# Kernel tuning notes

Measured on AMD Instinct MI355X. Metric: run time of the kernel, lower is better.

Reference implementation:

```python
import jax, jax.numpy as jnp
import numpy as np

M = 64    # multiplicity (channels per harmonic degree)
P = 64    # positional encoding dim
EPS = 1e-5


def sinusoidal_pe(N, P):
    pos = jnp.arange(N, dtype=jnp.float32)[:, None]
    div = jnp.exp(jnp.arange(0, P, 2, dtype=jnp.float32) * (-np.log(10000.0) / P))
    pe = jnp.zeros((N, P), dtype=jnp.float32)
    pe = pe.at[:, 0::2].set(jnp.sin(pos * div))
    pe = pe.at[:, 1::2].set(jnp.cos(pos * div))
    return pe


def split_irreps(h):
    # h: [B, N, 4M] -> scalar part [B,N,M], vector part [B,N,M,3]
    B, N, _ = h.shape
    h4 = h.reshape(B, N, M, 4)
    return h4[..., 0], h4[..., 1:]


def merge_irreps(s, v):
    B, N, _ = s.shape
    return jnp.concatenate([s[..., None], v], axis=-1).reshape(B, N, M * 4)


def hyena_block(h, Wq, Wk, Wv, filt, Wo):
    # Hyena-style gated long convolution: q * conv(k * v), FFT circular conv along seq
    N = h.shape[1]
    q = h @ Wq
    k = h @ Wk
    v = h @ Wv
    kf = jnp.fft.rfft(filt, n=N, axis=0)                       # [N//2+1, H]
    conv = jnp.fft.irfft(jnp.fft.rfft(k * v, n=N, axis=1) * kf[None], n=N, axis=1)
    return (q * conv) @ Wo


def reg_linear(h, W0, W1):
    # degree-wise linear mixing across multiplicity (equivariant)
    s, v = split_irreps(h)
    return merge_irreps(jnp.einsum('bnm,mk->bnk', s, W0),
                        jnp.einsum('bnmd,mk->bnkd', v, W1))


def reg_batchnorm(h, g0, g1):
    # normalize per-channel irrep norms over (batch, tokens); learnable per-channel gain
    s, v = split_irreps(h)
    n0 = jnp.sqrt(jnp.mean(s * s, axis=(0, 1)) + EPS)          # [M]
    n1 = jnp.sqrt(jnp.mean(jnp.sum(v * v, axis=-1), axis=(0, 1)) + EPS)
    return merge_irreps(s / n0 * g0, v / n1[:, None] * g1[:, None])


def norm_activation(h):
    # norm-gated nonlinearity: each irrep scaled by sigmoid of its norm (equivariant)
    s, v = split_irreps(h)
    vn = jnp.sqrt(jnp.sum(v * v, axis=-1, keepdims=True) + EPS)
    return merge_irreps(s * jax.nn.sigmoid(jnp.abs(s)), v * jax.nn.sigmoid(vn))


def setup_inputs() -> dict:
    key = jax.random.key(0)
    B, N = 64, 1024
    D = M * 4
    H = [360, 360, 160]   # 10*sum(2l+1,l<=5)=360, 360, 10*sum(2l+1,l<=3)=160
    ks = iter(jax.random.split(key, 64))
    def rn(shape, scale=0.02):
        return jax.random.normal(next(ks), shape, dtype=jnp.float32) * scale
    inp = {
        'x': jax.random.normal(next(ks), (B, N, 3), dtype=jnp.float32),
        'tok_emb': rn((3, P)),
        'Wf': rn((P, M)),
        'wv': rn((M,), 0.5),
        'w_out': rn((M,), 0.5),
    }
    for i, Hi in enumerate(H, start=1):
        inp[f'Wq{i}'] = rn((D, Hi)); inp[f'Wk{i}'] = rn((D, Hi)); inp[f'Wv{i}'] = rn((D, Hi))
        inp[f'filt{i}'] = rn((N, Hi)); inp[f'Wo{i}'] = rn((Hi, D))
        inp[f'Wm0_{i}'] = rn((M, M)); inp[f'Wm1_{i}'] = rn((M, M))
        inp[f'g0_{i}'] = jnp.ones((M,), jnp.float32); inp[f'g1_{i}'] = jnp.ones((M,), jnp.float32)
    return inp


def reference(x, tok_emb, Wf, wv, w_out,
              Wq1, Wk1, Wv1, filt1, Wo1, Wm0_1, Wm1_1, g0_1, g1_1,
              Wq2, Wk2, Wv2, filt2, Wo2, Wm0_2, Wm1_2, g0_2, g1_2,
              Wq3, Wk3, Wv3, filt3, Wo3, Wm0_3, Wm1_3, g0_3, g1_3):
    B, N, _ = x.shape
    # invariant features: sinusoidal PE + token-type embedding (alternating 0/1, last token 2)
    pe = sinusoidal_pe(N, P)
    tt = jnp.arange(N) % 2
    tt = tt.at[-1].set(2)
    f = pe + tok_emb[tt]                                        # [N, P]
    # input conversion: invariants -> degree-0 channels; input vector -> degree-1 channels
    s0 = jnp.broadcast_to((f @ Wf)[None], (B, N, M))
    v0 = x[:, :, None, :] * wv[None, None, :, None]             # [B, N, M, 3]
    h = merge_irreps(s0, v0)                                    # [B, N, 4M]
    layers = [
        (Wq1, Wk1, Wv1, filt1, Wo1, Wm0_1, Wm1_1, g0_1, g1_1),
        (Wq2, Wk2, Wv2, filt2, Wo2, Wm0_2, Wm1_2, g0_2, g1_2),
        (Wq3, Wk3, Wv3, filt3, Wo3, Wm0_3, Wm1_3, g0_3, g1_3),
    ]
    for (Wq, Wk, Wv_, filt, Wo, Wm0, Wm1, g0, g1) in layers:
        h = h + hyena_block(h, Wq, Wk, Wv_, filt, Wo)           # hyena + residual
        y = reg_linear(h, Wm0, Wm1)                             # mlp
        y = reg_batchnorm(y, g0, g1)                            # batch norm
        y = norm_activation(y)                                  # norm activation
        h = h + y                                               # residual
    pooled = h.mean(axis=1)                                     # [B, 4M] mean pool over tokens
    _, vpool = split_irreps(pooled[:, None, :])                 # [B, 1, M, 3]
    return jnp.einsum('bmd,m->bd', vpool[:, 0], w_out)          # [B, 3]
```

## Files before the change

kernel.cpp:

```cpp
#include <hip/hip_runtime.h>
#include <math.h>

namespace {

typedef __bf16 bf16_t;
typedef bf16_t bf16x8 __attribute__((ext_vector_type(8)));
typedef float floatx4 __attribute__((ext_vector_type(4)));

constexpr int kN = 1024;
constexpr int kM = 64;
constexpr int kP = 64;
constexpr float kEps = 1e-5f;
constexpr int kFN = 1024;

__device__ __forceinline__ float sigmoidf(float v) { return 1.0f / (1.0f + expf(-v)); }

__device__ __forceinline__ floatx4 mfma16(bf16x8 a, bf16x8 b, floatx4 c) {
  return __builtin_amdgcn_mfma_f32_16x16x32_bf16(a, b, c, 0, 0, 0);
}

__device__ __forceinline__ void fma3(floatx4& acc, bf16x8 ah, bf16x8 al,
                                     bf16x8 bh, bf16x8 bl) {
  acc = mfma16(ah, bh, acc);
  acc = mfma16(ah, bl, acc);
  acc = mfma16(al, bh, acc);
}

__device__ __forceinline__ void load_split8(const float* p, bf16x8& hi, bf16x8& lo) {
  const float4 u = *(const float4*)p;
  const float4 v = *(const float4*)(p + 4);
  const float a[8] = {u.x, u.y, u.z, u.w, v.x, v.y, v.z, v.w};
#pragma unroll
  for (int i = 0; i < 8; ++i) {
    const bf16_t h_ = (bf16_t)a[i];
    hi[i] = h_;
    lo[i] = (bf16_t)(a[i] - (float)h_);
  }
}

union U4 { uint4 u; bf16_t b[8]; };

__device__ __forceinline__ void glds16(const bf16_t* g, bf16_t* l) {
  __builtin_amdgcn_global_load_lds(
      (const __attribute__((address_space(1))) void*)g,
      (__attribute__((address_space(3))) void*)l, 16, 0, 0);
}

__device__ __forceinline__ size_t hidx(int r, int d8) {
  const int rb = r >> 6, rr = r & 63;
  return (size_t)(rb * 8 + (d8 >> 2)) * 4096 + (rr >> 4) * 1024 + (d8 & 3) * 128 + (rr & 15) * 8;
}

__device__ __forceinline__ int zi(int i) { return i + (i >> 4); }

__device__ __forceinline__ float2 cadd(float2 a, float2 b) { return {a.x + b.x, a.y + b.y}; }
__device__ __forceinline__ float2 csub(float2 a, float2 b) { return {a.x - b.x, a.y - b.y}; }
__device__ __forceinline__ float2 cmul(float2 a, float2 w) {
  return {a.x * w.x - a.y * w.y, a.x * w.y + a.y * w.x};
}
__device__ __forceinline__ float2 cmulc(float2 a, float2 w) {
  return {a.x * w.x + a.y * w.y, a.y * w.x - a.x * w.y};
}

__global__ void k_s0(const float* __restrict__ tok_emb, const float* __restrict__ Wf,
                     float* __restrict__ s0) {
  __shared__ float f[kP];
  const int n = blockIdx.x;
  const int t = threadIdx.x;
  const int tt = (n == kN - 1) ? 2 : (n & 1);
  const int j = t >> 1;
  const float cexp = (float)(-9.210340371976184 / 64.0);
  const float divj = expf((float)(2 * j) * cexp);
  const float ang = (float)n * divj;
  const float pe = (t & 1) ? cosf(ang) : sinf(ang);
  f[t] = pe + tok_emb[tt * kP + t];
  __syncthreads();
  float acc = 0.0f;
#pragma unroll 8
  for (int p = 0; p < kP; ++p) acc = fmaf(f[p], Wf[p * kM + t], acc);
  s0[n * kM + t] = acc;
}

__global__ void k_h0(const float* __restrict__ x, const float* __restrict__ wv,
                     const float* __restrict__ s0, bf16_t* __restrict__ hsh) {
  const int idx = blockIdx.x * 256 + threadIdx.x;
  const int r = idx >> 5, d8 = idx & 31;
  const int n = r & (kN - 1);
  const int m0 = d8 * 2, m1 = m0 + 1;
  const float w0 = wv[m0], w1 = wv[m1];
  const float x0 = x[r * 3 + 0], x1 = x[r * 3 + 1], x2 = x[r * 3 + 2];
  float f[8];
  f[0] = s0[n * kM + m0]; f[1] = x0 * w0; f[2] = x1 * w0; f[3] = x2 * w0;
  f[4] = s0[n * kM + m1]; f[5] = x0 * w1; f[6] = x1 * w1; f[7] = x2 * w1;
  U4 oh, ol;
#pragma unroll
  for (int i = 0; i < 8; ++i) {
    const bf16_t h_ = (bf16_t)f[i];
    oh.b[i] = h_; ol.b[i] = (bf16_t)(f[i] - (float)h_);
  }
  const size_t base = hidx(r, d8);
  *(uint4*)(hsh + base) = oh.u;
  *(uint4*)(hsh + base + 512) = ol.u;
}

__global__ void k_wqkv3(const float* __restrict__ Wq0, const float* __restrict__ Wk0,
                        const float* __restrict__ Wv0,
                        const float* __restrict__ Wq1, const float* __restrict__ Wk1,
                        const float* __restrict__ Wv1,
                        const float* __restrict__ Wq2, const float* __restrict__ Wk2,
                        const float* __restrict__ Wv2, bf16_t* __restrict__ wall3) {
  const int l = blockIdx.y;
  const int H = (l == 2) ? 160 : 360;
  const int gy = (l == 2) ? 3 : 6;
  const int c = blockIdx.x;
  if (c >= gy * 64) return;
  const int k = threadIdx.x;
  const float* Wq = (l == 0) ? Wq0 : ((l == 1) ? Wq1 : Wq2);
  const float* Wk = (l == 0) ? Wk0 : ((l == 1) ? Wk1 : Wk2);
  const float* Wv = (l == 0) ? Wv0 : ((l == 1) ? Wv1 : Wv2);
  bf16_t* wall = wall3 + ((l == 2) ? 1179648 : (size_t)l * 589824);
  const bool ok = c < H;
  const float w[3] = {ok ? Wq[k * H + c] : 0.f, ok ? Wk[k * H + c] : 0.f,
                      ok ? Wv[k * H + c] : 0.f};
  const int ct = c >> 6, cgrp = (c >> 4) & 3, cl = c & 15;
  const int kc = k >> 5, quad = (k >> 3) & 3, off = k & 7;
  const size_t base = (size_t)(ct * 8 + kc) * 12288 + cgrp * 512 + quad * 128 + cl * 8 + off;
#pragma unroll
  for (int mat = 0; mat < 3; ++mat) {
    const bf16_t hi = (bf16_t)w[mat];
    wall[base + mat * 4096] = hi;
    wall[base + mat * 4096 + 2048] = (bf16_t)(w[mat] - (float)hi);
  }
}

__global__ void k_wo3(const float* __restrict__ Wo0, const float* __restrict__ Wo1,
                      const float* __restrict__ Wo2, bf16_t* __restrict__ WoF3) {
  const int l = blockIdx.y;
  const int H = (l == 2) ? 160 : 360;
  const float* Wo = (l == 0) ? Wo0 : ((l == 1) ? Wo1 : Wo2);
  bf16_t* WoF = WoF3 + (size_t)l * 196608;
  const int d = blockIdx.x;
  const int c = threadIdx.x;
  const float w = (c < H) ? Wo[c * 256 + d] : 0.f;
  const int dt = d >> 6, dgrp = (d >> 4) & 3, dl = d & 15;
  const int kc = c >> 5, quad = (c >> 3) & 3, off = c & 7;
  const size_t base = (size_t)(dt * 12 + kc) * 4096 + dgrp * 512 + quad * 128 + dl * 8 + off;
  const bf16_t hi = (bf16_t)w;
  WoF[base] = hi;
  WoF[base + 2048] = (bf16_t)(w - (float)hi);
}

__global__ void k_bt3(const float* __restrict__ W00, const float* __restrict__ W10,
                      const float* __restrict__ W01, const float* __restrict__ W11,
                      const float* __restrict__ W02, const float* __restrict__ W12,
                      bf16_t* __restrict__ BtF3) {
  const int l = blockIdx.y;
  const float* W0 = (l == 0) ? W00 : ((l == 1) ? W01 : W02);
  const float* W1 = (l == 0) ? W10 : ((l == 1) ? W11 : W12);
  bf16_t* BtF = BtF3 + (size_t)l * 131072;
  const int col = blockIdx.x, row = threadIdx.x;
  const int k = col >> 2, ck = col & 3, m = row >> 2, cm = row & 3;
  float v = 0.f;
  if (cm == ck) v = (ck == 0 ? W0 : W1)[m * 64 + k];
  const int ct = col >> 6, cgrp = (col >> 4) & 3, cl = col & 15;
  const int kc = row >> 5, quad = (row >> 3) & 3, off = row & 7;
  const size_t base = (size_t)(ct * 8 + kc) * 4096 + cgrp * 512 + quad * 128 + cl * 8 + off;
  const bf16_t hi = (bf16_t)v;
  BtF[base] = hi;
  BtF[base + 2048] = (bf16_t)(v - (float)hi);
}

__global__ void k_tw(float2* __restrict__ twg) {
  const int j = blockIdx.x * 256 + threadIdx.x;
  if (j < kFN / 2) {
    float s, c;
    sincosf(-6.283185307179586f * (float)j / (float)kFN, &s, &c);
    twg[j].x = c; twg[j].y = s;
  }
}

__device__ void fft_dif(float2* z, const float2* tw) {
  const int p = threadIdx.x;
#pragma unroll
  for (int m = 256; m >= 1; m >>= 2) {
    __syncthreads();
    const int pm = p & (m - 1);
    const int j = ((p & ~(m - 1)) << 2) | pm;
    const int tm2 = 512 / (2 * m), tm1 = 512 / m;
    const float2 x0 = z[zi(j)], x1 = z[zi(j + m)];
    const float2 x2 = z[zi(j + 2 * m)], x3 = z[zi(j + 3 * m)];
    const float2 w2 = tw[pm * tm2], w2b = tw[(pm + m) * tm2], w1 = tw[pm * tm1];
    const float2 a0 = cadd(x0, x2), a2 = cmul(csub(x0, x2), w2);
    const float2 a1 = cadd(x1, x3), a3 = cmul(csub(x1, x3), w2b);
    z[zi(j)]         = cadd(a0, a1);
    z[zi(j + m)]     = cmul(csub(a0, a1), w1);
    z[zi(j + 2 * m)] = cadd(a2, a3);
    z[zi(j + 3 * m)] = cmul(csub(a2, a3), w1);
  }
}

__device__ void fft_dit_inv(float2* z, const float2* tw) {
  const int p = threadIdx.x;
#pragma unroll
  for (int m = 1; m <= 256; m <<= 2) {
    __syncthreads();
    const int pm = p & (m - 1);
    const int j = ((p & ~(m - 1)) << 2) | pm;
    const int tm2 = 512 / (2 * m), tm1 = 512 / m;
    const float2 x0 = z[zi(j)], x1 = z[zi(j + m)];
    const float2 x2 = z[zi(j + 2 * m)], x3 = z[zi(j + 3 * m)];
    const float2 w1 = tw[pm * tm1], w2 = tw[pm * tm2], w2b = tw[(pm + m) * tm2];
    const float2 c1 = cmulc(x1, w1), c3 = cmulc(x3, w1);
    const float2 b0 = cadd(x0, c1), b1 = csub(x0, c1);
    const float2 b2 = cadd(x2, c3), b3 = csub(x2, c3);
    const float2 d2 = cmulc(b2, w2), d3 = cmulc(b3, w2b);
    z[zi(j)]         = cadd(b0, d2);
    z[zi(j + 2 * m)] = csub(b0, d2);
    z[zi(j + m)]     = cadd(b1, d3);
    z[zi(j + 3 * m)] = csub(b1, d3);
  }
}

__global__ __launch_bounds__(256) void k_kf(const float* __restrict__ filt, int H,
                                            const float2* __restrict__ twg,
                                            float2* __restrict__ kf) {
  __shared__ float2 z[kFN + kFN / 16];
  __shared__ float2 tw[kFN / 2];
  const int c = blockIdx.x;
  for (int j = threadIdx.x; j < kFN / 2; j += 256) tw[j] = twg[j];
  for (int n = threadIdx.x; n < kFN; n += 256) {
    z[zi(n)].x = filt[n * H + c];
    z[zi(n)].y = 0.0f;
  }
  fft_dif(z, tw);
  __syncthreads();
  for (int j = threadIdx.x; j < kFN; j += 256) kf[c * kFN + j] = z[zi(j)];
}

__global__ __launch_bounds__(256) void k_conv(float* kvt, const float* __restrict__ qt,
                                              const float2* __restrict__ kf,
                                              const float2* __restrict__ twg, int H) {
  __shared__ float2 z[kFN + kFN / 16];
  __shared__ float2 tw[kFN / 2];
  const int blk = blockIdx.x;
  const int c = blk % H;
  const int pb = blk / H;
  float* sig0 = kvt + (((size_t)((2 * pb) * H + c)) << 10);
  float* sig1 = kvt + (((size_t)((2 * pb + 1) * H + c)) << 10);
  const float* q0 = qt + (((size_t)((2 * pb) * H + c)) << 10);
  const float* q1 = qt + (((size_t)((2 * pb + 1) * H + c)) << 10);
  for (int j = threadIdx.x; j < kFN / 2; j += 256) tw[j] = twg[j];
  for (int n = threadIdx.x; n < kFN; n += 256) {
    z[zi(n)].x = sig0[n];
    z[zi(n)].y = sig1[n];
  }
  fft_dif(z, tw);
  __syncthreads();
  for (int j = threadIdx.x; j < kFN; j += 256) {
    const float2 a = z[zi(j)];
    const float2 b = kf[c * kFN + j];
    float2 o;
    o.x = a.x * b.x - a.y * b.y;
    o.y = a.x * b.y + a.y * b.x;
    z[zi(j)] = o;
  }
  fft_dit_inv(z, tw);
  __syncthreads();
  const float s = 1.0f / (float)kFN;
  for (int n = threadIdx.x; n < kFN; n += 256) {
    sig0[n] = (z[zi(n)].x * s) * q0[n];
    sig1[n] = (z[zi(n)].y * s) * q1[n];
  }
}

__global__ __launch_bounds__(256) void k_qkv(const bf16_t* __restrict__ hsh,
    const bf16_t* __restrict__ wall, int H,
    float* __restrict__ qt, float* __restrict__ kvt) {
  __shared__ bf16_t lds[20480];
  const int gy = (H + 63) >> 6;
  const int bid = blockIdx.x;
  const int xcd = bid & 7, sseq = bid >> 3;
  const int ct = sseq % gy;
  const int rb2 = (sseq / gy) * 8 + xcd;
  const int rb0 = rb2 * 2, rb1 = rb0 + 1;
  const int t = threadIdx.x;
  const int lane = t & 63, wave = t >> 6;
  const int l15 = lane & 15, quad = lane >> 4;
  const int c0 = ct * 64;
  const int wr = (wave & 1) * 32, wc = (wave >> 1) * 32;
  const int wr16 = (wave & 1) * 2, wc16 = (wave >> 1) * 2;
  const int q128l = quad * 128 + l15 * 8;
  floatx4 aq[2][2][2] = {}, ak_[2][2][2] = {}, av_[2][2][2] = {};
  for (int kt = 0; kt < 8; ++kt) {
    {
      const bf16_t* A0 = hsh + (size_t)(rb0 * 8 + kt) * 4096;
      const bf16_t* A1 = hsh + (size_t)(rb1 * 8 + kt) * 4096;
      const bf16_t* Bs = wall + (size_t)(ct * 8 + kt) * 12288;
#pragma unroll
      for (int s = 0; s < 10; ++s) {
        const int seg = wave * 10 + s;
        const bf16_t* src = (seg < 8) ? (A0 + seg * 512)
                          : (seg < 16) ? (A1 + (seg - 8) * 512)
                                       : (Bs + (seg - 16) * 512);
        glds16(src + lane * 8, &lds[seg * 512]);
      }
    }
    __syncthreads();
    bf16x8 ah[2][2], al[2][2];
#pragma unroll
    for (int rbx = 0; rbx < 2; ++rbx)
#pragma unroll
      for (int i = 0; i < 2; ++i) {
        ah[rbx][i] = *(const bf16x8*)(lds + rbx * 4096 + ((wr16 + i) * 2 + 0) * 512 + q128l);
        al[rbx][i] = *(const bf16x8*)(lds + rbx * 4096 + ((wr16 + i) * 2 + 1) * 512 + q128l);
      }
#pragma unroll
    for (int mat = 0; mat < 3; ++mat) {
      const int bb = 8192 + mat * 4096;
#pragma unroll
      for (int j = 0; j < 2; ++j) {
        const bf16x8 bh = *(const bf16x8*)(lds + bb + (wc16 + j) * 512 + q128l);
        const bf16x8 bl = *(const bf16x8*)(lds + bb + 2048 + (wc16 + j) * 512 + q128l);
#pragma unroll
        for (int rbx = 0; rbx < 2; ++rbx)
#pragma unroll
          for (int i = 0; i < 2; ++i) {
            floatx4& a = (mat == 0) ? aq[rbx][i][j]
                       : (mat == 1) ? ak_[rbx][i][j] : av_[rbx][i][j];
            fma3(a, ah[rbx][i], al[rbx][i], bh, bl);
          }
      }
    }
    __syncthreads();
  }
#pragma unroll
  for (int rbx = 0; rbx < 2; ++rbx) {
    const int r0 = (rb0 + rbx) * 64;
    const int b = r0 >> 10;
    const int n0 = r0 & 1023;
#pragma unroll
    for (int j = 0; j < 2; ++j) {
      const int c = c0 + wc + j * 16 + l15;
      if (c < H) {
        const size_t rbw = (((size_t)(b * H + c)) << 10) + n0 + wr + quad * 4;
#pragma unroll
        for (int i = 0; i < 2; ++i) {
          float4 p;
          p.x = aq[rbx][i][j][0]; p.y = aq[rbx][i][j][1];
          p.z = aq[rbx][i][j][2]; p.w = aq[rbx][i][j][3];
          *(float4*)(qt + rbw + i * 16) = p;
        }
#pragma unroll
        for (int i = 0; i < 2; ++i) {
          float4 p;
          p.x = ak_[rbx][i][j][0] * av_[rbx][i][j][0];
          p.y = ak_[rbx][i][j][1] * av_[rbx][i][j][1];
          p.z = ak_[rbx][i][j][2] * av_[rbx][i][j][2];
          p.w = ak_[rbx][i][j][3] * av_[rbx][i][j][3];
          *(float4*)(kvt + rbw + i * 16) = p;
        }
      }
    }
  }
}

__global__ __launch_bounds__(256) void k_mix(const float* __restrict__ pv, int H, int KT,
    const bf16_t* __restrict__ WoF, bf16_t* __restrict__ hsh) {
  __shared__ float smem[4352];
  const int r0 = blockIdx.x * 64;
  const int t = threadIdx.x;
  const int lane = t & 63, wave = t >> 6;
  const int l15 = lane & 15, quad = lane >> 4;
  const int b = r0 >> 10, n0 = r0 & 1023;
  const int wr = (wave & 1) * 32, wh = wave >> 1;
  const int q128l = quad * 128 + l15 * 8;
  floatx4 acc[2][8] = {};
  const int cl = t >> 3, n8 = (t & 7) * 8;
  for (int kt = 0; kt < KT; ++kt) {
    const int ck0 = kt * 32;
    __syncthreads();
    {
      const int c = ck0 + cl;
      float p[8] = {};
      if (c < H) {
        const size_t o = (((size_t)(b * H + c)) << 10) + n0 + n8;
        const float4 p0 = *(const float4*)(pv + o);
        const float4 p1 = *(const float4*)(pv + o + 4);
        p[0] = p0.x; p[1] = p0.y; p[2] = p0.z; p[3] = p0.w;
        p[4] = p1.x; p[5] = p1.y; p[6] = p1.z; p[7] = p1.w;
      }
#pragma unroll
      for (int u = 0; u < 8; ++u) smem[(n8 + u) * 36 + cl] = p[u];
    }
    __syncthreads();
    bf16x8 ah0, al0, ah1, al1;
    load_split8(smem + (wr + l15) * 36 + quad * 8, ah0, al0);
    load_split8(smem + (wr + 16 + l15) * 36 + quad * 8, ah1, al1);
#pragma unroll
    for (int j = 0; j < 8; ++j) {
      const int jj = wh * 8 + j;
      const int dt = jj >> 2, dgrp = jj & 3;
      const bf16_t* Bb = WoF + (size_t)(dt * 12 + kt) * 4096 + dgrp * 512 + q128l;
      const bf16x8 bh = *(const bf16x8*)Bb;
      const bf16x8 bl = *(const bf16x8*)(Bb + 2048);
      fma3(acc[0][j], ah0, al0, bh, bl);
      fma3(acc[1][j], ah1, al1, bh, bl);
    }
  }
  const int nl = t >> 2, q4 = t & 3;
  const int r = r0 + nl;
#pragma unroll
  for (int g = 0; g < 4; ++g) {
    __syncthreads();
    if (wh == (g >> 1)) {
#pragma unroll
      for (int jl = 0; jl < 4; ++jl) {
        const int j = (g & 1) * 4 + jl;
#pragma unroll
        for (int i = 0; i < 2; ++i)
#pragma unroll
          for (int rr = 0; rr < 4; ++rr)
            smem[(wr + i * 16 + quad * 4 + rr) * 68 + jl * 16 + l15] = acc[i][j][rr];
      }
    }
    __syncthreads();
#pragma unroll
    for (int u8 = 0; u8 < 2; ++u8) {
      const int d8 = g * 8 + q4 * 2 + u8;
      const size_t base = hidx(r, d8);
      U4 hi, lo;
      hi.u = *(const uint4*)(hsh + base);
      lo.u = *(const uint4*)(hsh + base + 512);
      U4 oh, ol;
#pragma unroll
      for (int i = 0; i < 8; ++i) {
        const float f = (float)hi.b[i] + (float)lo.b[i] +
                        smem[nl * 68 + (q4 * 2 + u8) * 8 + i];
        const bf16_t h_ = (bf16_t)f;
        oh.b[i] = h_; ol.b[i] = (bf16_t)(f - (float)h_);
      }
      *(uint4*)(hsh + base) = oh.u;
      *(uint4*)(hsh + base + 512) = ol.u;
    }
  }
}

__global__ __launch_bounds__(256) void k_reg(const bf16_t* __restrict__ hsh,
    const bf16_t* __restrict__ BtF,
    float* __restrict__ y, float* __restrict__ partial) {
  __shared__ float smf[6144];
  __shared__ float red[256];
  bf16_t* lds = (bf16_t*)smf;
  const int bid = blockIdx.x;
  const int xcd = bid & 7, sseq = bid >> 3;
  const int ct = sseq & 3;
  const int rb2 = (sseq >> 2) * 8 + xcd;
  const int rb0 = rb2 * 2, rb1 = rb0 + 1;
  const int t = threadIdx.x;
  const int lane = t & 63, wave = t >> 6;
  const int l15 = lane & 15, quad = lane >> 4;
  const int c0 = ct * 64;
  const int wr = (wave & 1) * 32, wc = (wave >> 1) * 32;
  const int wr16 = (wave & 1) * 2, wc16 = (wave >> 1) * 2;
  const int q128l = quad * 128 + l15 * 8;
  floatx4 acc[2][2][2] = {};
  for (int kt = 0; kt < 8; ++kt) {
    {
      const bf16_t* A0 = hsh + (size_t)(rb0 * 8 + kt) * 4096;
      const bf16_t* A1 = hsh + (size_t)(rb1 * 8 + kt) * 4096;
      const bf16_t* Bs = BtF + (size_t)(ct * 8 + kt) * 4096;
#pragma unroll
      for (int s = 0; s < 6; ++s) {
        const int seg = wave * 6 + s;
        const bf16_t* src = (seg < 8) ? (A0 + seg * 512)
                          : (seg < 16) ? (A1 + (seg - 8) * 512)
                                       : (Bs + (seg - 16) * 512);
        glds16(src + lane * 8, &lds[seg * 512]);
      }
    }
    __syncthreads();
    bf16x8 ah[2][2], al[2][2];
#pragma unroll
    for (int rbx = 0; rbx < 2; ++rbx)
#pragma unroll
      for (int i = 0; i < 2; ++i) {
        ah[rbx][i] = *(const bf16x8*)(lds + rbx * 4096 + ((wr16 + i) * 2 + 0) * 512 + q128l);
        al[rbx][i] = *(const bf16x8*)(lds + rbx * 4096 + ((wr16 + i) * 2 + 1) * 512 + q128l);
      }
#pragma unroll
    for (int j = 0; j < 2; ++j) {
      const bf16x8 bh = *(const bf16x8*)(lds + 8192 + (wc16 + j) * 512 + q128l);
      const bf16x8 bl = *(const bf16x8*)(lds + 8192 + 2048 + (wc16 + j) * 512 + q128l);
#pragma unroll
      for (int rbx = 0; rbx < 2; ++rbx)
#pragma unroll
        for (int i = 0; i < 2; ++i)
          fma3(acc[rbx][i][j], ah[rbx][i], al[rbx][i], bh, bl);
    }
    __syncthreads();
  }
#pragma unroll
  for (int rbx = 0; rbx < 2; ++rbx)
#pragma unroll
    for (int j = 0; j < 2; ++j) {
      float s = 0.f;
#pragma unroll
      for (int i = 0; i < 2; ++i)
#pragma unroll
        for (int r = 0; r < 4; ++r)
          s = fmaf(acc[rbx][i][j][r], acc[rbx][i][j][r], s);
      s += __shfl_down(s, 32);
      s += __shfl_down(s, 16);
      if (lane < 16) red[rbx * 128 + wave * 32 + j * 16 + lane] = s;
    }
#pragma unroll
  for (int rbx = 0; rbx < 2; ++rbx) {
    __syncthreads();
#pragma unroll
    for (int i = 0; i < 2; ++i)
#pragma unroll
      for (int j = 0; j < 2; ++j)
#pragma unroll
        for (int r = 0; r < 4; ++r)
          smf[(wr + i * 16 + quad * 4 + r) * 68 + wc + j * 16 + l15] = acc[rbx][i][j][r];
    __syncthreads();
    const int nl = t >> 2, q4 = t & 3;
    const int r0 = (rb0 + rbx) * 64;
    const size_t gi = (size_t)(r0 + nl) * 256 + c0 + q4 * 16;
#pragma unroll
    for (int u = 0; u < 4; ++u) {
      float4 yv;
      yv.x = smf[nl * 68 + q4 * 16 + u * 4 + 0];
      yv.y = smf[nl * 68 + q4 * 16 + u * 4 + 1];
      yv.z = smf[nl * 68 + q4 * 16 + u * 4 + 2];
      yv.w = smf[nl * 68 + q4 * 16 + u * 4 + 3];
      *(float4*)(y + gi + u * 4) = yv;
    }
  }
  if (t < 64) {
    const int w0 = (t >= 32) ? 2 : 0;
    const float v0 = red[w0 * 32 + (t & 31)] + red[(w0 + 1) * 32 + (t & 31)];
    const float v1 = red[128 + w0 * 32 + (t & 31)] + red[128 + (w0 + 1) * 32 + (t & 31)];
    partial[(size_t)rb0 * 256 + c0 + t] = v0;
    partial[(size_t)rb1 * 256 + c0 + t] = v1;
  }
}

__global__ __launch_bounds__(256) void k_stat(const float* __restrict__ partial,
                                              float* __restrict__ st) {
  __shared__ float sm1[16][16];
  __shared__ float tot[16];
  const int bb = blockIdx.x;
  const int t = threadIdx.x;
  const int col16 = t & 15, rgrp = t >> 4;
  const int c = bb * 16 + col16;
  float s = 0.f;
  for (int r = rgrp; r < 1024; r += 16) s += partial[(size_t)r * 256 + c];
  sm1[rgrp][col16] = s;
  __syncthreads();
  if (t < 16) {
    float v = 0.f;
#pragma unroll
    for (int g = 0; g < 16; ++g) v += sm1[g][t];
    tot[t] = v;
  }
  __syncthreads();
  if (t < 4) {
    const int m = bb * 4 + t;
    st[m] = tot[4 * t];
    st[64 + m] = tot[4 * t + 1] + tot[4 * t + 2] + tot[4 * t + 3];
  }
}

__global__ void k_bnact(const float* __restrict__ y, const float* __restrict__ stats,
    const float* __restrict__ g0, const float* __restrict__ g1, bf16_t* __restrict__ hsh) {
  const int idx = blockIdx.x * 256 + threadIdx.x;
  const int r = idx >> 5, d8 = idx & 31;
  const int m0 = d8 * 2, m1 = m0 + 1;
  const float i00 = g0[m0] / sqrtf(stats[m0] * (1.0f / 65536.0f) + kEps);
  const float i10 = g1[m0] / sqrtf(stats[64 + m0] * (1.0f / 65536.0f) + kEps);
  const float i01 = g0[m1] / sqrtf(stats[m1] * (1.0f / 65536.0f) + kEps);
  const float i11 = g1[m1] / sqrtf(stats[64 + m1] * (1.0f / 65536.0f) + kEps);
  const float* yr = y + (size_t)r * 256 + d8 * 8;
  const float4 ya = *(const float4*)yr;
  const float4 yb = *(const float4*)(yr + 4);
  float a[8];
  {
    const float s = ya.x * i00;
    const float vx = ya.y * i10, vy = ya.z * i10, vz = ya.w * i10;
    const float so = s * sigmoidf(fabsf(s));
    const float vn = sqrtf(fmaf(vx, vx, fmaf(vy, vy, vz * vz)) + kEps);
    const float gv = sigmoidf(vn);
    a[0] = so; a[1] = vx * gv; a[2] = vy * gv; a[3] = vz * gv;
  }
  {
    const float s = yb.x * i01;
    const float vx = yb.y * i11, vy = yb.z * i11, vz = yb.w * i11;
    const float so = s * sigmoidf(fabsf(s));
    const float vn = sqrtf(fmaf(vx, vx, fmaf(vy, vy, vz * vz)) + kEps);
    const float gv = sigmoidf(vn);
    a[4] = so; a[5] = vx * gv; a[6] = vy * gv; a[7] = vz * gv;
  }
  const size_t base = hidx(r, d8);
  U4 hi, lo;
  hi.u = *(const uint4*)(hsh + base);
  lo.u = *(const uint4*)(hsh + base + 512);
  U4 oh, ol;
#pragma unroll
  for (int i = 0; i < 8; ++i) {
    const float f = (float)hi.b[i] + (float)lo.b[i] + a[i];
    const bf16_t h_ = (bf16_t)f;
    oh.b[i] = h_; ol.b[i] = (bf16_t)(f - (float)h_);
  }
  *(uint4*)(hsh + base) = oh.u;
  *(uint4*)(hsh + base + 512) = ol.u;
}

__global__ __launch_bounds__(256) void k_pool(const bf16_t* __restrict__ hsh,
    const float* __restrict__ w_out, float* __restrict__ out) {
  __shared__ float r0s[256], r1s[256], r2s[256];
  const int b = blockIdx.x;
  const int t = threadIdx.x;
  float p0 = 0, p1 = 0, p2 = 0;
  for (int idx = t; idx < kN * 32; idx += 256) {
    const int n = idx >> 5, d8 = idx & 31;
    const int r = (b << 10) + n;
    const size_t base = hidx(r, d8);
    U4 hi, lo;
    hi.u = *(const uint4*)(hsh + base);
    lo.u = *(const uint4*)(hsh + base + 512);
    const float w0 = w_out[d8 * 2], w1 = w_out[d8 * 2 + 1];
    p0 += ((float)hi.b[1] + (float)lo.b[1]) * w0 + ((float)hi.b[5] + (float)lo.b[5]) * w1;
    p1 += ((float)hi.b[2] + (float)lo.b[2]) * w0 + ((float)hi.b[6] + (float)lo.b[6]) * w1;
    p2 += ((float)hi.b[3] + (float)lo.b[3]) * w0 + ((float)hi.b[7] + (float)lo.b[7]) * w1;
  }
  r0s[t] = p0; r1s[t] = p1; r2s[t] = p2;
  __syncthreads();
  for (int s = 128; s > 0; s >>= 1) {
    if (t < s) { r0s[t] += r0s[t + s]; r1s[t] += r1s[t + s]; r2s[t] += r2s[t + s]; }
    __syncthreads();
  }
  if (t == 0) {
    out[b * 3 + 0] = r0s[0] * (1.0f / kN);
    out[b * 3 + 1] = r1s[0] * (1.0f / kN);
    out[b * 3 + 2] = r2s[0] * (1.0f / kN);
  }
}

}

extern "C" void kernel_launch(void* const* d_in, const int* in_sizes, int n_in,
                              void* d_out, int out_size, void* d_ws, size_t ws_size,
                              hipStream_t stream) {
  const float* x       = (const float*)d_in[0];
  const float* tok_emb = (const float*)d_in[1];
  const float* Wf      = (const float*)d_in[2];
  const float* wv      = (const float*)d_in[3];
  const float* w_out   = (const float*)d_in[4];

  float* ws    = (float*)d_ws;
  bf16_t* hsh  = (bf16_t*)ws;
  float*  kvt  = ws + 16777216;
  float*  qt   = kvt + 23592960;
  float*  y    = qt;
  float*  partial = qt + 20000000;
  float*  s0   = qt + 23592960;
  float*  kf   = s0 + 65536;
  bf16_t* wall3 = (bf16_t*)(kf + 737280);
  bf16_t* WoF3  = wall3 + 1474560;
  bf16_t* BtF3  = WoF3 + 589824;
  float* stats = (float*)(BtF3 + 393216);
  float* twg   = stats + 384;

  k_tw<<<2, 256, 0, stream>>>((float2*)twg);
  k_s0<<<kN, 64, 0, stream>>>(tok_emb, Wf, s0);
  k_h0<<<8192, 256, 0, stream>>>(x, wv, s0, hsh);
  k_wqkv3<<<dim3(384, 3), 256, 0, stream>>>(
      (const float*)d_in[5], (const float*)d_in[6], (const float*)d_in[7],
      (const float*)d_in[14], (const float*)d_in[15], (const float*)d_in[16],
      (const float*)d_in[23], (const float*)d_in[24], (const float*)d_in[25], wall3);
  k_wo3<<<dim3(256, 3), 384, 0, stream>>>(
      (const float*)d_in[9], (const float*)d_in[18], (const float*)d_in[27], WoF3);
  k_bt3<<<dim3(256, 3), 256, 0, stream>>>(
      (const float*)d_in[10], (const float*)d_in[11],
      (const float*)d_in[19], (const float*)d_in[20],
      (const float*)d_in[28], (const float*)d_in[29], BtF3);

  for (int l = 0; l < 3; ++l) {
    const float* filt = (const float*)d_in[5 + 9 * l + 3];
    const float* g0   = (const float*)d_in[5 + 9 * l + 7];
    const float* g1   = (const float*)d_in[5 + 9 * l + 8];
    const int H = (l == 2) ? 160 : 360;
    const int gy = (H + 63) / 64;
    const int KT = gy * 2;
    bf16_t* wall = wall3 + ((l == 2) ? 1179648 : (size_t)l * 589824);
    bf16_t* WoF  = WoF3 + (size_t)l * 196608;
    bf16_t* BtF  = BtF3 + (size_t)l * 131072;
    float* st = stats + l * 128;

    k_kf<<<H, 256, 0, stream>>>(filt, H, (const float2*)twg, (float2*)kf);
    k_qkv<<<gy * 512, 256, 0, stream>>>(hsh, wall, H, qt, kvt);
    k_conv<<<32 * H, 256, 0, stream>>>(kvt, qt, (const float2*)kf, (const float2*)twg, H);
    k_mix<<<1024, 256, 0, stream>>>(kvt, H, KT, WoF, hsh);
    k_reg<<<2048, 256, 0, stream>>>(hsh, BtF, y, partial);
    k_stat<<<16, 256, 0, stream>>>(partial, st);
    k_bnact<<<8192, 256, 0, stream>>>(y, st, g0, g1, hsh);
  }

  k_pool<<<64, 256, 0, stream>>>(hsh, w_out, (float*)d_out);
}
```

Baseline: 1.275 ms.

## Store q and k*v intermediates in bf16 and batch filter FFTs once

k_qkv now writes q and k*v as single bf16 instead of fp32, and k_conv reads these bf16 buffers and writes the gated product to a separate fp32 buffer. This roughly halves the memory traffic of the large intermediate tensors between the projection and FFT-convolution kernels. The filter FFTs for all three layers are computed in one launch up front instead of one launch per layer. The BN input y is stored as a bf16 hi/lo pair, which keeps its bytes the same. Dropping q and k*v to plain bf16 loses precision compared with the prior fp32 path and may affect accuracy.

```diff
diff --git a/kernel.cpp b/kernel.cpp
--- a/kernel.cpp
+++ b/kernel.cpp
@@ -12,6 +12,7 @@
 constexpr int kP = 64;
 constexpr float kEps = 1e-5f;
 constexpr int kFN = 1024;
+constexpr size_t kYOFF = 16777216;
 
 __device__ __forceinline__ float sigmoidf(float v) { return 1.0f / (1.0f + expf(-v)); }
 
@@ -39,6 +40,8 @@
 }
 
 union U4 { uint4 u; bf16_t b[8]; };
+union Pk4 { uint2 u; bf16_t b[4]; };
+union Ub2 { uint u; bf16_t b[2]; };
 
 __device__ __forceinline__ void glds16(const bf16_t* g, bf16_t* l) {
   __builtin_amdgcn_global_load_lds(
@@ -221,12 +224,17 @@
   }
 }
 
-__global__ __launch_bounds__(256) void k_kf(const float* __restrict__ filt, int H,
-                                            const float2* __restrict__ twg,
-                                            float2* __restrict__ kf) {
+__global__ __launch_bounds__(256) void k_kf3(const float* __restrict__ f0,
+    const float* __restrict__ f1, const float* __restrict__ f2,
+    const float2* __restrict__ twg, float2* __restrict__ kf3) {
   __shared__ float2 z[kFN + kFN / 16];
   __shared__ float2 tw[kFN / 2];
-  const int c = blockIdx.x;
+  const int bid = blockIdx.x;
+  const int l = (bid < 360) ? 0 : ((bid < 720) ? 1 : 2);
+  const int c = bid - ((l == 0) ? 0 : ((l == 1) ? 360 : 720));
+  const int H = (l == 2) ? 160 : 360;
+  const float* filt = (l == 0) ? f0 : ((l == 1) ? f1 : f2);
+  float2* kf = kf3 + (size_t)l * 368640;
   for (int j = threadIdx.x; j < kFN / 2; j += 256) tw[j] = twg[j];
   for (int n = threadIdx.x; n < kFN; n += 256) {
     z[zi(n)].x = filt[n * H + c];
@@ -237,22 +245,23 @@
   for (int j = threadIdx.x; j < kFN; j += 256) kf[c * kFN + j] = z[zi(j)];
 }
 
-__global__ __launch_bounds__(256) void k_conv(float* kvt, const float* __restrict__ qt,
-                                              const float2* __restrict__ kf,
-                                              const float2* __restrict__ twg, int H) {
+__global__ __launch_bounds__(256) void k_conv(const bf16_t* __restrict__ kvb,
+    const bf16_t* __restrict__ qb, float* __restrict__ prod,
+    const float2* __restrict__ kf, const float2* __restrict__ twg, int H) {
   __shared__ float2 z[kFN + kFN / 16];
   __shared__ float2 tw[kFN / 2];
   const int blk = blockIdx.x;
   const int c = blk % H;
   const int pb = blk / H;
-  float* sig0 = kvt + (((size_t)((2 * pb) * H + c)) << 10);
-  float* sig1 = kvt + (((size_t)((2 * pb + 1) * H + c)) << 10);
-  const float* q0 = qt + (((size_t)((2 * pb) * H + c)) << 10);
-  const float* q1 = qt + (((size_t)((2 * pb + 1) * H + c)) << 10);
+  const size_t off0 = ((size_t)((2 * pb) * H + c)) << 10;
+  const size_t off1 = ((size_t)((2 * pb + 1) * H + c)) << 10;
   for (int j = threadIdx.x; j < kFN / 2; j += 256) tw[j] = twg[j];
-  for (int n = threadIdx.x; n < kFN; n += 256) {
-    z[zi(n)].x = sig0[n];
-    z[zi(n)].y = sig1[n];
+  for (int n2 = threadIdx.x; n2 < 512; n2 += 256) {
+    Ub2 a0, a1;
+    a0.u = *(const uint*)(kvb + off0 + 2 * n2);
+    a1.u = *(const uint*)(kvb + off1 + 2 * n2);
+    z[zi(2 * n2)].x = (float)a0.b[0];     z[zi(2 * n2)].y = (float)a1.b[0];
+    z[zi(2 * n2 + 1)].x = (float)a0.b[1]; z[zi(2 * n2 + 1)].y = (float)a1.b[1];
   }
   fft_dif(z, tw);
   __syncthreads();
@@ -267,15 +276,23 @@
   fft_dit_inv(z, tw);
   __syncthreads();
   const float s = 1.0f / (float)kFN;
-  for (int n = threadIdx.x; n < kFN; n += 256) {
-    sig0[n] = (z[zi(n)].x * s) * q0[n];
-    sig1[n] = (z[zi(n)].y * s) * q1[n];
+  for (int n2 = threadIdx.x; n2 < 512; n2 += 256) {
+    Ub2 q0, q1;
+    q0.u = *(const uint*)(qb + off0 + 2 * n2);
+    q1.u = *(const uint*)(qb + off1 + 2 * n2);
+    float2 p0, p1;
+    p0.x = (z[zi(2 * n2)].x * s) * (float)q0.b[0];
+    p0.y = (z[zi(2 * n2 + 1)].x * s) * (float)q0.b[1];
+    p1.x = (z[zi(2 * n2)].y * s) * (float)q1.b[0];
+    p1.y = (z[zi(2 * n2 + 1)].y * s) * (float)q1.b[1];
+    *(float2*)(prod + off0 + 2 * n2) = p0;
+    *(float2*)(prod + off1 + 2 * n2) = p1;
   }
 }
 
 __global__ __launch_bounds__(256) void k_qkv(const bf16_t* __restrict__ hsh,
     const bf16_t* __restrict__ wall, int H,
-    float* __restrict__ qt, float* __restrict__ kvt) {
+    bf16_t* __restrict__ qtb, bf16_t* __restrict__ kvb) {
   __shared__ bf16_t lds[20480];
   const int gy = (H + 63) >> 6;
   const int bid = blockIdx.x;
@@ -345,19 +362,14 @@
         const size_t rbw = (((size_t)(b * H + c)) << 10) + n0 + wr + quad * 4;
 #pragma unroll
         for (int i = 0; i < 2; ++i) {
-          float4 p;
-          p.x = aq[rbx][i][j][0]; p.y = aq[rbx][i][j][1];
-          p.z = aq[rbx][i][j][2]; p.w = aq[rbx][i][j][3];
-          *(float4*)(qt + rbw + i * 16) = p;
-        }
-#pragma unroll
-        for (int i = 0; i < 2; ++i) {
-          float4 p;
-          p.x = ak_[rbx][i][j][0] * av_[rbx][i][j][0];
-          p.y = ak_[rbx][i][j][1] * av_[rbx][i][j][1];
-          p.z = ak_[rbx][i][j][2] * av_[rbx][i][j][2];
-          p.w = ak_[rbx][i][j][3] * av_[rbx][i][j][3];
-          *(float4*)(kvt + rbw + i * 16) = p;
+          Pk4 pq, pk;
+#pragma unroll
+          for (int r = 0; r < 4; ++r) {
+            pq.b[r] = (bf16_t)aq[rbx][i][j][r];
+            pk.b[r] = (bf16_t)(ak_[rbx][i][j][r] * av_[rbx][i][j][r]);
+          }
+          *(uint2*)(qtb + rbw + i * 16) = pq.u;
+          *(uint2*)(kvb + rbw + i * 16) = pk.u;
         }
       }
     }
@@ -447,7 +459,7 @@
 
 __global__ __launch_bounds__(256) void k_reg(const bf16_t* __restrict__ hsh,
     const bf16_t* __restrict__ BtF,
-    float* __restrict__ y, float* __restrict__ partial) {
+    bf16_t* __restrict__ ybf, float* __restrict__ partial) {
   __shared__ float smf[6144];
   __shared__ float red[256];
   bf16_t* lds = (bf16_t*)smf;
@@ -528,13 +540,16 @@
     const int r0 = (rb0 + rbx) * 64;
     const size_t gi = (size_t)(r0 + nl) * 256 + c0 + q4 * 16;
 #pragma unroll
-    for (int u = 0; u < 4; ++u) {
-      float4 yv;
-      yv.x = smf[nl * 68 + q4 * 16 + u * 4 + 0];
-      yv.y = smf[nl * 68 + q4 * 16 + u * 4 + 1];
-      yv.z = smf[nl * 68 + q4 * 16 + u * 4 + 2];
-      yv.w = smf[nl * 68 + q4 * 16 + u * 4 + 3];
-      *(float4*)(y + gi + u * 4) = yv;
+    for (int u2 = 0; u2 < 2; ++u2) {
+      U4 oh, ol;
+#pragma unroll
+      for (int i = 0; i < 8; ++i) {
+        const float f = smf[nl * 68 + q4 * 16 + u2 * 8 + i];
+        const bf16_t h_ = (bf16_t)f;
+        oh.b[i] = h_; ol.b[i] = (bf16_t)(f - (float)h_);
+      }
+      *(uint4*)(ybf + gi + u2 * 8) = oh.u;
+      *(uint4*)(ybf + kYOFF + gi + u2 * 8) = ol.u;
     }
   }
   if (t < 64) {
@@ -572,7 +587,7 @@
   }
 }
 
-__global__ void k_bnact(const float* __restrict__ y, const float* __restrict__ stats,
+__global__ void k_bnact(const bf16_t* __restrict__ ybf, const float* __restrict__ stats,
     const float* __restrict__ g0, const float* __restrict__ g1, bf16_t* __restrict__ hsh) {
   const int idx = blockIdx.x * 256 + threadIdx.x;
   const int r = idx >> 5, d8 = idx & 31;
@@ -581,21 +596,25 @@
   const float i10 = g1[m0] / sqrtf(stats[64 + m0] * (1.0f / 65536.0f) + kEps);
   const float i01 = g0[m1] / sqrtf(stats[m1] * (1.0f / 65536.0f) + kEps);
   const float i11 = g1[m1] / sqrtf(stats[64 + m1] * (1.0f / 65536.0f) + kEps);
-  const float* yr = y + (size_t)r * 256 + d8 * 8;
-  const float4 ya = *(const float4*)yr;
-  const float4 yb = *(const float4*)(yr + 4);
+  const size_t ye = (size_t)r * 256 + d8 * 8;
+  U4 yh, yl;
+  yh.u = *(const uint4*)(ybf + ye);
+  yl.u = *(const uint4*)(ybf + kYOFF + ye);
+  float yv[8];
+#pragma unroll
+  for (int i = 0; i < 8; ++i) yv[i] = (float)yh.b[i] + (float)yl.b[i];
   float a[8];
   {
-    const float s = ya.x * i00;
-    const float vx = ya.y * i10, vy = ya.z * i10, vz = ya.w * i10;
+    const float s = yv[0] * i00;
+    const float vx = yv[1] * i10, vy = yv[2] * i10, vz = yv[3] * i10;
     const float so = s * sigmoidf(fabsf(s));
     const float vn = sqrtf(fmaf(vx, vx, fmaf(vy, vy, vz * vz)) + kEps);
     const float gv = sigmoidf(vn);
     a[0] = so; a[1] = vx * gv; a[2] = vy * gv; a[3] = vz * gv;
   }
   {
-    const float s = yb.x * i01;
-    const float vx = yb.y * i11, vy = yb.z * i11, vz = yb.w * i11;
+    const float s = yv[4] * i01;
+    const float vx = yv[5] * i11, vy = yv[6] * i11, vz = yv[7] * i11;
     const float so = s * sigmoidf(fabsf(s));
     const float vn = sqrtf(fmaf(vx, vx, fmaf(vy, vy, vz * vz)) + kEps);
     const float gv = sigmoidf(vn);
@@ -660,13 +679,14 @@
 
   float* ws    = (float*)d_ws;
   bf16_t* hsh  = (bf16_t*)ws;
-  float*  kvt  = ws + 16777216;
-  float*  qt   = kvt + 23592960;
-  float*  y    = qt;
-  float*  partial = qt + 20000000;
-  float*  s0   = qt + 23592960;
-  float*  kf   = s0 + 65536;
-  bf16_t* wall3 = (bf16_t*)(kf + 737280);
+  bf16_t* kvb  = (bf16_t*)(ws + 16777216);
+  bf16_t* qtb  = (bf16_t*)(ws + 28573696);
+  float*  prod = ws + 40370176;
+  bf16_t* ybf  = (bf16_t*)prod;
+  float*  partial = prod + 20000000;
+  float*  s0   = prod + 23592960;
+  float*  kf3  = s0 + 65536;
+  bf16_t* wall3 = (bf16_t*)(kf3 + 1802240);
   bf16_t* WoF3  = wall3 + 1474560;
   bf16_t* BtF3  = WoF3 + 589824;
   float* stats = (float*)(BtF3 + 393216);
@@ -685,9 +705,11 @@
       (const float*)d_in[10], (const float*)d_in[11],
       (const float*)d_in[19], (const float*)d_in[20],
       (const float*)d_in[28], (const float*)d_in[29], BtF3);
+  k_kf3<<<880, 256, 0, stream>>>(
+      (const float*)d_in[8], (const float*)d_in[17], (const float*)d_in[26],
+      (const float2*)twg, (float2*)kf3);
 
   for (int l = 0; l < 3; ++l) {
-    const float* filt = (const float*)d_in[5 + 9 * l + 3];
     const float* g0   = (const float*)d_in[5 + 9 * l + 7];
     const float* g1   = (const float*)d_in[5 + 9 * l + 8];
     const int H = (l == 2) ? 160 : 360;
@@ -696,15 +718,15 @@
     bf16_t* wall = wall3 + ((l == 2) ? 1179648 : (size_t)l * 589824);
     bf16_t* WoF  = WoF3 + (size_t)l * 196608;
     bf16_t* BtF  = BtF3 + (size_t)l * 131072;
+    const float2* kf = (const float2*)kf3 + (size_t)l * 368640;
     float* st = stats + l * 128;
 
-    k_kf<<<H, 256, 0, stream>>>(filt, H, (const float2*)twg, (float2*)kf);
-    k_qkv<<<gy * 512, 256, 0, stream>>>(hsh, wall, H, qt, kvt);
-    k_conv<<<32 * H, 256, 0, stream>>>(kvt, qt, (const float2*)kf, (const float2*)twg, H);
-    k_mix<<<1024, 256, 0, stream>>>(kvt, H, KT, WoF, hsh);
-    k_reg<<<2048, 256, 0, stream>>>(hsh, BtF, y, partial);
+    k_qkv<<<gy * 512, 256, 0, stream>>>(hsh, wall, H, qtb, kvb);
+    k_conv<<<32 * H, 256, 0, stream>>>(kvb, qtb, prod, kf, (const float2*)twg, H);
+    k_mix<<<1024, 256, 0, stream>>>(prod, H, KT, WoF, hsh);
+    k_reg<<<2048, 256, 0, stream>>>(hsh, BtF, ybf, partial);
     k_stat<<<16, 256, 0, stream>>>(partial, st);
-    k_bnact<<<8192, 256, 0, stream>>>(y, st, g0, g1, hsh);
+    k_bnact<<<8192, 256, 0, stream>>>(ybf, st, g0, g1, hsh);
   }
 
   k_pool<<<64, 256, 0, stream>>>(hsh, w_out, (float*)d_out);
```

Measured after the change: 1.192 ms. -6.5%, faster.
